# Performance work log

Hardware: AMD Instinct MI355X
Metric: run time of the kernel (lower is better)

## Reference

```python
import jax, jax.numpy as jnp
import numpy as np

CONF_THRES = 0.25
IOU_THRES = 0.45
MAX_DET = 300
K_NMS = 2048          # static candidate cap for jit-compatible NMS
MAX_WH = 7680.0       # yolov5 class-offset trick for non-agnostic NMS
IN_H, IN_W = 640.0, 640.0     # network input size (self.size)
OUT_H, OUT_W = 1080.0, 1920.0  # original frame size (h, w)


def setup_inputs() -> dict:
    key = jax.random.key(0)
    k1, k2, k3, k4 = jax.random.split(key, 4)
    bs, n, nc = 16, 25200, 80
    # realistic raw yolov5 head output: xywh in pixels, obj/cls in [0,1]
    xy = jax.random.uniform(k1, (bs, n, 2), jnp.float32) * 640.0
    wh = jax.random.uniform(k2, (bs, n, 2), jnp.float32) * 120.0 + 2.0
    obj = jax.random.uniform(k3, (bs, n, 1), jnp.float32)
    cls = jax.random.uniform(k4, (bs, n, nc), jnp.float32)
    preds = jnp.concatenate([xy, wh, obj, cls], axis=-1)  # [bs, 25200, 85]
    return {"preds": preds}


def _xywh2xyxy(x):
    xy, wh = x[..., :2], x[..., 2:4]
    return jnp.concatenate([xy - wh * 0.5, xy + wh * 0.5], axis=-1)


def _iou_one_many(b, boxes):
    # b: [4], boxes: [K,4] (xyxy) -> [K]
    lt = jnp.maximum(b[:2], boxes[:, :2])
    rb = jnp.minimum(b[2:], boxes[:, 2:])
    wh = jnp.clip(rb - lt, 0.0)
    inter = wh[:, 0] * wh[:, 1]
    a1 = (b[2] - b[0]) * (b[3] - b[1])
    a2 = (boxes[:, 2] - boxes[:, 0]) * (boxes[:, 3] - boxes[:, 1])
    return inter / (a1 + a2 - inter + 1e-7)


def _nms_sorted(boxes, valid):
    # boxes [K,4] sorted by score desc (class-offset applied); valid [K] bool
    K = boxes.shape[0]
    idxs = jnp.arange(K)

    def step(suppressed, i):
        keep_i = valid[i] & jnp.logical_not(suppressed[i])
        iou = _iou_one_many(boxes[i], boxes)  # [K]
        suppressed = suppressed | (keep_i & (iou > IOU_THRES) & (idxs > i))
        return suppressed, keep_i

    _, keep = jax.lax.scan(step, jnp.zeros((K,), bool), idxs)
    # first MAX_DET kept indices (stable: preserves score order)
    sel = jnp.argsort(jnp.logical_not(keep), stable=True)[:MAX_DET]
    return sel, keep[sel]


def reference(preds):
    # --- yolov5 non_max_suppression (multi_label=False, agnostic=False) ---
    obj = preds[..., 4:5]                      # [bs,N,1]
    cls_conf = preds[..., 5:] * obj            # conf = obj * cls
    conf = jnp.max(cls_conf, axis=-1)          # [bs,N]
    cls = jnp.argmax(cls_conf, axis=-1)        # [bs,N] int
    mask = (preds[..., 4] > CONF_THRES) & (conf > CONF_THRES)
    score = jnp.where(mask, conf, -1.0)

    top_s, top_i = jax.lax.top_k(score, K_NMS)                      # [bs,K]
    cand_xywh = jnp.take_along_axis(preds[..., :4], top_i[..., None], axis=1)
    cand_boxes = _xywh2xyxy(cand_xywh)                              # [bs,K,4]
    cand_cls = jnp.take_along_axis(cls, top_i, axis=1)              # [bs,K]
    valid = top_s > 0.0

    boxes_off = cand_boxes + cand_cls[..., None].astype(cand_boxes.dtype) * MAX_WH
    sel, keep = jax.vmap(_nms_sorted)(boxes_off, valid)             # [bs,MAX_DET]

    det_boxes = jnp.take_along_axis(cand_boxes, sel[..., None], axis=1)
    det_scores = jnp.take_along_axis(top_s, sel, axis=1)
    det_cls = jnp.take_along_axis(cand_cls, sel, axis=1)

    # --- scale_bbox: (640,640) -> (h,w) original frame ---
    scale = jnp.array([OUT_W / IN_W, OUT_H / IN_H, OUT_W / IN_W, OUT_H / IN_H],
                      dtype=det_boxes.dtype)
    det_boxes = det_boxes * scale

    det = jnp.concatenate(
        [det_boxes, det_scores[..., None], det_cls[..., None].astype(det_boxes.dtype)],
        axis=-1)                                                    # [bs,MAX_DET,6]
    det = jnp.where(keep[..., None], det, 0.0)
    return det
```

## Files before the change

### kernel.cpp

```cpp
#include <hip/hip_runtime.h>
#include <stdint.h>

#define BS 16
#define NP 25200
#define NC 80
#define DIM 85
#define KN 2048
#define CAP 4096
#define BINS 512
#define MAXD 300
#define NBLK 394

__global__ __launch_bounds__(256) void score_kernel(const float* __restrict__ preds,
        float* __restrict__ score, int* __restrict__ clsout) {
    int b = blockIdx.x / NBLK;
    int blk = blockIdx.x % NBLK;
    int i0 = blk * 64;
    int nb = min(64, NP - i0);
    __shared__ float4 s4[64 * DIM / 4];
    const float4* p4 = (const float4*)(preds + ((size_t)b * NP + i0) * DIM);
    int tot4 = (nb * DIM) >> 2;
    float4 tmp[6];
    #pragma unroll
    for (int kx = 0; kx < 6; ++kx) {
        int idx = kx * 256 + threadIdx.x;
        tmp[kx] = (idx < tot4) ? p4[idx] : make_float4(0.f, 0.f, 0.f, 0.f);
    }
    #pragma unroll
    for (int kx = 0; kx < 6; ++kx) {
        int idx = kx * 256 + threadIdx.x;
        if (idx < tot4) s4[idx] = tmp[kx];
    }
    __syncthreads();
    const float* s = (const float*)s4;
    int box = threadIdx.x >> 2, sub = threadIdx.x & 3;
    if (box < nb) {
        const float* bp = s + box * DIM;
        float obj = bp[4];
        float best = -1.0f; int bidx = sub * 20;
        #pragma unroll
        for (int c = 0; c < 20; ++c) {
            float v = bp[5 + sub * 20 + c] * obj;
            if (v > best) { best = v; bidx = sub * 20 + c; }
        }
        #pragma unroll
        for (int off = 1; off < 4; off <<= 1) {
            float ob = __shfl_xor(best, off);
            int   oi = __shfl_xor(bidx, off);
            if (ob > best || (ob == best && oi < bidx)) { best = ob; bidx = oi; }
        }
        if (sub == 0) {
            bool m = (obj > 0.25f) && (best > 0.25f);
            int gi = b * NP + i0 + box;
            score[gi] = m ? best : -1.0f;
            clsout[gi] = bidx;
        }
    }
}

template<int V, bool DESC, typename T>
__device__ inline void wave_bitonic(T (&v)[V], int lane) {
    const int N = V * 64;
    #pragma unroll
    for (int k = 2; k <= N; k <<= 1) {
        #pragma unroll
        for (int j = N >> 1; j > 0; j >>= 1) {
            if (j >= k) continue;
            if (j >= 64) {
                int dv = j >> 6;
                #pragma unroll
                for (int a = 0; a < V; ++a) {
                    int p = a ^ dv;
                    if (a < p) {
                        int e = a * 64;
                        bool kml = (((e & k) == 0) == DESC);
                        T lo = v[a], hi = v[p];
                        T mx = lo > hi ? lo : hi;
                        T mn = lo > hi ? hi : lo;
                        v[a] = kml ? mx : mn;
                        v[p] = kml ? mn : mx;
                    }
                }
            } else {
                #pragma unroll
                for (int a = 0; a < V; ++a) {
                    int e = a * 64 + lane;
                    T pv = __shfl_xor(v[a], j);
                    bool isLower = (lane & j) == 0;
                    bool kml = (((e & k) == 0) == DESC);
                    bool takeMax = (kml == isLower);
                    T mx = v[a] > pv ? v[a] : pv;
                    T mn = v[a] > pv ? pv : v[a];
                    v[a] = takeMax ? mx : mn;
                }
            }
        }
    }
}

__global__ __launch_bounds__(1024) void sort_kernel(
        const float* __restrict__ score, const float* __restrict__ preds,
        const int* __restrict__ cls,
        unsigned long long* __restrict__ gkeys, float4* __restrict__ gboxes,
        int* __restrict__ gcarr, unsigned short* __restrict__ gcorder,
        int* __restrict__ gcstart, int* __restrict__ gccnt,
        unsigned char* __restrict__ keepG) {
    int b = blockIdx.x;
    int tid = threadIdx.x;
    int lane = tid & 63;
    int wid = tid >> 6;

    __shared__ unsigned long long k[CAP];
    __shared__ int h[BINS];
    __shared__ int bstartA[BINS];
    __shared__ int bcnt[BINS];
    __shared__ int carr[KN];
    __shared__ unsigned short corder[KN];
    __shared__ int sT;

    for (int t = tid; t < BINS; t += 1024) { h[t] = 0; bcnt[t] = 0; }
    __syncthreads();
    const float* sb = score + (size_t)b * NP;
    for (int i = tid; i < NP; i += 1024) {
        float v = sb[i];
        if (v > 0.0f) {
            int bin = (int)(__float_as_uint(v) >> 15) - 0x7D00;
            bin = max(0, min(BINS - 1, bin));
            atomicAdd(&h[bin], 1);
        }
    }
    __syncthreads();
    if (tid < 64) {
        int base = lane * 8;
        int v[8]; int ssum = 0;
        #pragma unroll
        for (int kk = 0; kk < 8; ++kk) { v[kk] = h[base + kk]; ssum += v[kk]; }
        int x = ssum;
        #pragma unroll
        for (int off = 1; off < 64; off <<= 1) {
            int y = __shfl_down(x, off);
            if (lane + off < 64) x += y;
        }
        int run = x - ssum;
        int cand = -1;
        #pragma unroll
        for (int kk = 7; kk >= 0; --kk) {
            bstartA[base + kk] = run;
            run += v[kk];
            if (run >= KN && cand < 0) cand = base + kk;
        }
        #pragma unroll
        for (int off = 1; off < 64; off <<= 1) cand = max(cand, __shfl_xor(cand, off));
        if (lane == 0) sT = max(cand, 0);
    }
    __syncthreads();
    int T = sT;
    int n = min(bstartA[T] + h[T], CAP);
    int Mb = min(n, KN);
    for (int i = tid; i < NP; i += 1024) {
        float sc = sb[i];
        if (sc > 0.0f) {
            int bin = (int)(__float_as_uint(sc) >> 15) - 0x7D00;
            bin = max(0, min(BINS - 1, bin));
            if (bin >= T) {
                int pos = bstartA[bin] + atomicAdd(&bcnt[bin], 1);
                if (pos < CAP) {
                    unsigned int ii = (unsigned int)i;
                    k[pos] = ((unsigned long long)__float_as_uint(sc) << 32)
                           | (unsigned int)(~ii);
                }
            }
        }
    }
    __syncthreads();
    for (int bin = (T & ~15) + wid; bin < BINS; bin += 16) {
        if (bin < T) continue;
        int cnt = h[bin];
        if (cnt <= 0) continue;
        int bs = bstartA[bin];
        unsigned long long v[4];
        #pragma unroll
        for (int a = 0; a < 4; ++a) {
            int idx = a * 64 + lane;
            v[a] = (idx < cnt && bs + idx < CAP) ? k[bs + idx] : 0ull;
        }
        wave_bitonic<4, true>(v, lane);
        #pragma unroll
        for (int a = 0; a < 4; ++a) {
            int idx = a * 64 + lane;
            if (idx < cnt && bs + idx < CAP) k[bs + idx] = v[a];
        }
    }
    __syncthreads();
    for (int r = tid; r < KN; r += 1024) {
        keepG[b * KN + r] = 0;
        if (r < Mb) {
            unsigned long long key = k[r];
            unsigned int i = ~(unsigned int)key;
            const float* p = preds + ((size_t)b * NP + i) * DIM;
            float x = p[0], y = p[1], w = p[2], hh = p[3];
            float4 bx = make_float4(x - w * 0.5f, y - hh * 0.5f,
                                    x + w * 0.5f, y + hh * 0.5f);
            int c = cls[(size_t)b * NP + i];
            gboxes[b * KN + r] = bx;
            gkeys [b * KN + r] = key;
            gcarr [b * KN + r] = c;
            carr[r] = c;
        }
    }
    if (tid < 128) { h[tid] = 0; bcnt[tid] = 0; }
    __syncthreads();
    for (int r = tid; r < Mb; r += 1024) atomicAdd(&h[carr[r]], 1);
    __syncthreads();
    if (tid < 64) {
        int a = h[lane];
        int sa = a;
        #pragma unroll
        for (int off = 1; off < 64; off <<= 1) {
            int y = __shfl_up(sa, off);
            if (lane >= off) sa += y;
        }
        bstartA[lane] = sa - a;
        int tot64 = __shfl(sa, 63);
        int b2 = (lane < 16) ? h[64 + lane] : 0;
        int sb2 = b2;
        #pragma unroll
        for (int off = 1; off < 64; off <<= 1) {
            int y = __shfl_up(sb2, off);
            if (lane >= off) sb2 += y;
        }
        if (lane < 16) bstartA[64 + lane] = tot64 + (sb2 - b2);
    }
    __syncthreads();
    for (int r = tid; r < Mb; r += 1024) {
        int c = carr[r];
        int pos = bstartA[c] + atomicAdd(&bcnt[c], 1);
        corder[pos] = (unsigned short)r;
    }
    __syncthreads();
    #pragma unroll
    for (int t5 = 0; t5 < 5; ++t5) {
        int c = wid + 16 * t5;
        int nc = h[c];
        int bs = bstartA[c];
        if (nc > 0) {
            unsigned int v[2];
            v[0] = (lane < nc) ? (unsigned int)corder[bs + lane] : 0xFFFFFFFFu;
            v[1] = (lane + 64 < nc) ? (unsigned int)corder[bs + 64 + lane] : 0xFFFFFFFFu;
            wave_bitonic<2, false>(v, lane);
            if (lane < nc) corder[bs + lane] = (unsigned short)v[0];
            if (lane + 64 < nc) corder[bs + 64 + lane] = (unsigned short)v[1];
        }
    }
    __syncthreads();
    for (int t = tid; t < Mb; t += 1024) gcorder[b * KN + t] = corder[t];
    if (tid < NC) { gcstart[b * NC + tid] = bstartA[tid]; gccnt[b * NC + tid] = h[tid]; }
}

__global__ __launch_bounds__(64) void nms_kernel(const float4* __restrict__ gboxes,
        const unsigned short* __restrict__ gcorder, const int* __restrict__ gcstart,
        const int* __restrict__ gccnt, unsigned char* __restrict__ keepG) {
    int b = blockIdx.x / NC;
    int c = blockIdx.x % NC;
    int nc = gccnt[b * NC + c];
    if (nc <= 0) return;
    int bs = gcstart[b * NC + c];
    int lane = threadIdx.x;
    int ord0 = (lane < nc) ? (int)gcorder[b * KN + bs + lane] : 0;
    int ord1 = (lane + 64 < nc) ? (int)gcorder[b * KN + bs + 64 + lane] : 0;
    float4 A0 = (lane < nc) ? gboxes[b * KN + ord0] : make_float4(0.f, 0.f, 0.f, 0.f);
    float4 A1 = (lane + 64 < nc) ? gboxes[b * KN + ord1] : make_float4(0.f, 0.f, 0.f, 0.f);
    float off = (float)c * 7680.0f;
    A0.x += off; A0.y += off; A0.z += off; A0.w += off;
    A1.x += off; A1.y += off; A1.z += off; A1.w += off;
    float ar0 = (A0.z - A0.x) * (A0.w - A0.y);
    float ar1 = (A1.z - A1.x) * (A1.w - A1.y);
    unsigned long long sup0 = 0, sup1 = 0, keep0 = 0, keep1 = 0;
    for (int idx = 0; idx < nc; ++idx) {
        bool hi = idx >= 64;
        int bit = idx & 63;
        unsigned long long s = hi ? sup1 : sup0;
        if ((s >> bit) & 1ull) continue;
        if (hi) keep1 |= 1ull << bit; else keep0 |= 1ull << bit;
        float bx_ = hi ? __shfl(A1.x, bit) : __shfl(A0.x, bit);
        float by_ = hi ? __shfl(A1.y, bit) : __shfl(A0.y, bit);
        float bz_ = hi ? __shfl(A1.z, bit) : __shfl(A0.z, bit);
        float bw_ = hi ? __shfl(A1.w, bit) : __shfl(A0.w, bit);
        float ba_ = hi ? __shfl(ar1, bit) : __shfl(ar0, bit);
        bool s0, s1;
        {
            float lx = fmaxf(bx_, A0.x), ly = fmaxf(by_, A0.y);
            float rx = fminf(bz_, A0.z), ry = fminf(bw_, A0.w);
            float iw = fmaxf(rx - lx, 0.0f), ih = fmaxf(ry - ly, 0.0f);
            float inter = iw * ih;
            float iou = inter / (ba_ + ar0 - inter + 1e-7f);
            s0 = (lane > idx) && (lane < nc) && (iou > 0.45f);
        }
        {
            float lx = fmaxf(bx_, A1.x), ly = fmaxf(by_, A1.y);
            float rx = fminf(bz_, A1.z), ry = fminf(bw_, A1.w);
            float iw = fmaxf(rx - lx, 0.0f), ih = fmaxf(ry - ly, 0.0f);
            float inter = iw * ih;
            float iou = inter / (ba_ + ar1 - inter + 1e-7f);
            s1 = ((64 + lane) > idx) && ((64 + lane) < nc) && (iou > 0.45f);
        }
        sup0 |= __ballot(s0);
        sup1 |= __ballot(s1);
    }
    if (lane < nc && ((keep0 >> lane) & 1ull)) keepG[b * KN + ord0] = 1;
    if (lane + 64 < nc && ((keep1 >> lane) & 1ull)) keepG[b * KN + ord1] = 1;
}

__global__ __launch_bounds__(64) void out_kernel(const unsigned char* __restrict__ keepG,
        const unsigned long long* __restrict__ gkeys, const float4* __restrict__ gboxes,
        const int* __restrict__ gcarr, float* __restrict__ out) {
    int b = blockIdx.x;
    int lane = threadIdx.x;
    int running = 0;
    for (int ch = 0; ch < 32; ++ch) {
        int r = ch * 64 + lane;
        bool kp = keepG[b * KN + r] != 0;
        unsigned long long m = __ballot(kp);
        int pos = running + (int)__popcll(m & ((1ull << lane) - 1ull));
        if (kp && pos < MAXD) {
            float4 bx = gboxes[b * KN + r];
            float sc = __uint_as_float((unsigned int)(gkeys[b * KN + r] >> 32));
            float* o = out + ((size_t)b * MAXD + pos) * 6;
            o[0] = bx.x * 3.0f;
            o[1] = bx.y * 1.6875f;
            o[2] = bx.z * 3.0f;
            o[3] = bx.w * 1.6875f;
            o[4] = sc;
            o[5] = (float)gcarr[b * KN + r];
        }
        running += (int)__popcll(m);
    }
}

extern "C" void kernel_launch(void* const* d_in, const int* in_sizes, int n_in,
                              void* d_out, int out_size, void* d_ws, size_t ws_size,
                              hipStream_t stream) {
    const float* preds = (const float*)d_in[0];
    float* out = (float*)d_out;
    char* ws = (char*)d_ws;
    size_t off = 0;
    auto alloc = [&](size_t bytes) -> void* {
        void* p = ws + off;
        off += (bytes + 255) & ~(size_t)255;
        return p;
    };
    float* score = (float*)alloc((size_t)BS * NP * 4);
    int* cls    = (int*)alloc((size_t)BS * NP * 4);
    unsigned long long* gkeys = (unsigned long long*)alloc((size_t)BS * KN * 8);
    float4* gboxes = (float4*)alloc((size_t)BS * KN * 16);
    int* gcarr  = (int*)alloc((size_t)BS * KN * 4);
    unsigned short* gcorder = (unsigned short*)alloc((size_t)BS * KN * 2);
    int* gcstart = (int*)alloc((size_t)BS * NC * 4);
    int* gccnt   = (int*)alloc((size_t)BS * NC * 4);
    unsigned char* keepG = (unsigned char*)alloc((size_t)BS * KN);
    if (ws_size < off) return;

    hipMemsetAsync(d_out, 0, (size_t)out_size * 4, stream);

    score_kernel<<<BS * NBLK, 256, 0, stream>>>(preds, score, cls);
    sort_kernel<<<BS, 1024, 0, stream>>>(score, preds, cls, gkeys, gboxes,
            gcarr, gcorder, gcstart, gccnt, keepG);
    nms_kernel<<<BS * NC, 64, 0, stream>>>(gboxes, gcorder, gcstart, gccnt, keepG);
    out_kernel<<<BS, 64, 0, stream>>>(keepG, gkeys, gboxes, gcarr, out);
}
```

Baseline: 292.8 us.

## Split sort stage across many blocks and fuse histogram into score kernel

The score kernel now computes the per-chunk score histogram and skips the class scan when objectness is below threshold. It also drops the shared-memory staging in favour of one thread per box. The single-block-per-image sort is split: a light kernel does the prefix and scatter to global keys, and a new multi-block kernel bitonic-sorts each bin and builds boxes. The per-class ordering moves into the NMS kernel, which compacts its own class members with a ballot scan. The aim is to remove the serial, low-occupancy 16-block sort bottleneck, at the cost of an extra launch, more global traffic, and uncoalesced per-thread strided reads of preds.

```diff
diff --git a/kernel.cpp b/kernel.cpp
--- a/kernel.cpp
+++ b/kernel.cpp
@@ -9,53 +9,50 @@
 #define CAP 4096
 #define BINS 512
 #define MAXD 300
-#define NBLK 394
-
-__global__ __launch_bounds__(256) void score_kernel(const float* __restrict__ preds,
-        float* __restrict__ score, int* __restrict__ clsout) {
-    int b = blockIdx.x / NBLK;
-    int blk = blockIdx.x % NBLK;
-    int i0 = blk * 64;
-    int nb = min(64, NP - i0);
-    __shared__ float4 s4[64 * DIM / 4];
-    const float4* p4 = (const float4*)(preds + ((size_t)b * NP + i0) * DIM);
-    int tot4 = (nb * DIM) >> 2;
-    float4 tmp[6];
-    #pragma unroll
-    for (int kx = 0; kx < 6; ++kx) {
-        int idx = kx * 256 + threadIdx.x;
-        tmp[kx] = (idx < tot4) ? p4[idx] : make_float4(0.f, 0.f, 0.f, 0.f);
-    }
-    #pragma unroll
-    for (int kx = 0; kx < 6; ++kx) {
-        int idx = kx * 256 + threadIdx.x;
-        if (idx < tot4) s4[idx] = tmp[kx];
-    }
-    __syncthreads();
-    const float* s = (const float*)s4;
-    int box = threadIdx.x >> 2, sub = threadIdx.x & 3;
-    if (box < nb) {
-        const float* bp = s + box * DIM;
+#define SBLK 99
+#define QCAP 128
+
+__global__ __launch_bounds__(256) void score_hist_kernel(const float* __restrict__ preds,
+        float* __restrict__ score, int* __restrict__ clsout, int* __restrict__ hpart) {
+    int b = blockIdx.x / SBLK;
+    int chunk = blockIdx.x % SBLK;
+    int tid = threadIdx.x;
+    __shared__ int h[BINS];
+    h[tid] = 0; h[tid + 256] = 0;
+    __syncthreads();
+    int n = chunk * 256 + tid;
+    if (n < NP) {
+        const float* bp = preds + ((size_t)b * NP + n) * DIM;
         float obj = bp[4];
-        float best = -1.0f; int bidx = sub * 20;
-        #pragma unroll
-        for (int c = 0; c < 20; ++c) {
-            float v = bp[5 + sub * 20 + c] * obj;
-            if (v > best) { best = v; bidx = sub * 20 + c; }
-        }
-        #pragma unroll
-        for (int off = 1; off < 4; off <<= 1) {
-            float ob = __shfl_xor(best, off);
-            int   oi = __shfl_xor(bidx, off);
-            if (ob > best || (ob == best && oi < bidx)) { best = ob; bidx = oi; }
-        }
-        if (sub == 0) {
-            bool m = (obj > 0.25f) && (best > 0.25f);
-            int gi = b * NP + i0 + box;
-            score[gi] = m ? best : -1.0f;
-            clsout[gi] = bidx;
-        }
-    }
+        float sc = -1.0f; int bidx = 0;
+        if (obj > 0.25f) {
+            float best = -1.0f;
+            #pragma unroll
+            for (int kk = 0; kk < 10; ++kk) {
+                float v[8];
+                #pragma unroll
+                for (int j = 0; j < 8; ++j) v[j] = bp[5 + kk * 8 + j];
+                #pragma unroll
+                for (int j = 0; j < 8; ++j) {
+                    float s = v[j] * obj;
+                    if (s > best) { best = s; bidx = kk * 8 + j; }
+                }
+            }
+            if (best > 0.25f) sc = best;
+        }
+        int gi = b * NP + n;
+        score[gi] = sc;
+        clsout[gi] = bidx;
+        if (sc > 0.0f) {
+            int bin = (int)(__float_as_uint(sc) >> 15) - 0x7D00;
+            bin = max(0, min(BINS - 1, bin));
+            atomicAdd(&h[bin], 1);
+        }
+    }
+    __syncthreads();
+    int* hp = hpart + ((size_t)(b * SBLK + chunk)) * BINS;
+    hp[tid] = h[tid];
+    hp[tid + 256] = h[tid + 256];
 }
 
 template<int V, bool DESC, typename T>
@@ -98,36 +95,24 @@
     }
 }
 
-__global__ __launch_bounds__(1024) void sort_kernel(
-        const float* __restrict__ score, const float* __restrict__ preds,
-        const int* __restrict__ cls,
-        unsigned long long* __restrict__ gkeys, float4* __restrict__ gboxes,
-        int* __restrict__ gcarr, unsigned short* __restrict__ gcorder,
-        int* __restrict__ gcstart, int* __restrict__ gccnt,
-        unsigned char* __restrict__ keepG) {
+__global__ __launch_bounds__(1024) void sort16_kernel(const float* __restrict__ score,
+        const int* __restrict__ hpart,
+        unsigned long long* __restrict__ gkeys, int* __restrict__ gmeta,
+        int* __restrict__ gbstart, int* __restrict__ gcnt,
+        unsigned char* __restrict__ carrU8, unsigned char* __restrict__ keepG) {
     int b = blockIdx.x;
     int tid = threadIdx.x;
     int lane = tid & 63;
-    int wid = tid >> 6;
-
-    __shared__ unsigned long long k[CAP];
     __shared__ int h[BINS];
     __shared__ int bstartA[BINS];
     __shared__ int bcnt[BINS];
-    __shared__ int carr[KN];
-    __shared__ unsigned short corder[KN];
     __shared__ int sT;
-
-    for (int t = tid; t < BINS; t += 1024) { h[t] = 0; bcnt[t] = 0; }
-    __syncthreads();
-    const float* sb = score + (size_t)b * NP;
-    for (int i = tid; i < NP; i += 1024) {
-        float v = sb[i];
-        if (v > 0.0f) {
-            int bin = (int)(__float_as_uint(v) >> 15) - 0x7D00;
-            bin = max(0, min(BINS - 1, bin));
-            atomicAdd(&h[bin], 1);
-        }
+    if (tid < BINS) {
+        int s = 0;
+        const int* hp = hpart + ((size_t)b * SBLK) * BINS + tid;
+        for (int c = 0; c < SBLK; ++c) s += hp[c * BINS];
+        h[tid] = s;
+        bcnt[tid] = 0;
     }
     __syncthreads();
     if (tid < 64) {
@@ -157,6 +142,7 @@
     int T = sT;
     int n = min(bstartA[T] + h[T], CAP);
     int Mb = min(n, KN);
+    const float* sb = score + (size_t)b * NP;
     for (int i = tid; i < NP; i += 1024) {
         float sc = sb[i];
         if (sc > 0.0f) {
@@ -166,108 +152,86 @@
                 int pos = bstartA[bin] + atomicAdd(&bcnt[bin], 1);
                 if (pos < CAP) {
                     unsigned int ii = (unsigned int)i;
-                    k[pos] = ((unsigned long long)__float_as_uint(sc) << 32)
-                           | (unsigned int)(~ii);
+                    gkeys[(size_t)b * CAP + pos] =
+                        ((unsigned long long)__float_as_uint(sc) << 32)
+                        | (unsigned int)(~ii);
                 }
             }
         }
     }
-    __syncthreads();
-    for (int bin = (T & ~15) + wid; bin < BINS; bin += 16) {
-        if (bin < T) continue;
-        int cnt = h[bin];
+    for (int r = tid; r < KN; r += 1024) { keepG[b * KN + r] = 0; carrU8[b * KN + r] = 0xFF; }
+    if (tid < BINS) { gbstart[b * BINS + tid] = bstartA[tid]; gcnt[b * BINS + tid] = h[tid]; }
+    if (tid == 0) { gmeta[2 * b] = T; gmeta[2 * b + 1] = Mb; }
+}
+
+__global__ __launch_bounds__(256) void binsort_build_kernel(const float* __restrict__ preds,
+        const int* __restrict__ cls, unsigned long long* __restrict__ gkeys,
+        const int* __restrict__ gmeta, const int* __restrict__ gbstart,
+        const int* __restrict__ gcnt,
+        float4* __restrict__ gboxes, unsigned char* __restrict__ carrU8) {
+    int b = blockIdx.x >> 5;
+    int g = blockIdx.x & 31;
+    int lane = threadIdx.x & 63;
+    int wv = threadIdx.x >> 6;
+    int T = gmeta[2 * b];
+    int Mb = gmeta[2 * b + 1];
+    int wslot = g * 4 + wv;
+    for (int bin = T + wslot; bin < BINS; bin += 128) {
+        int cnt = gcnt[b * BINS + bin];
         if (cnt <= 0) continue;
-        int bs = bstartA[bin];
+        int bs = gbstart[b * BINS + bin];
+        if (bs >= Mb) continue;
         unsigned long long v[4];
         #pragma unroll
         for (int a = 0; a < 4; ++a) {
             int idx = a * 64 + lane;
-            v[a] = (idx < cnt && bs + idx < CAP) ? k[bs + idx] : 0ull;
+            v[a] = (idx < cnt && bs + idx < CAP) ? gkeys[(size_t)b * CAP + bs + idx] : 0ull;
         }
         wave_bitonic<4, true>(v, lane);
         #pragma unroll
         for (int a = 0; a < 4; ++a) {
             int idx = a * 64 + lane;
-            if (idx < cnt && bs + idx < CAP) k[bs + idx] = v[a];
-        }
-    }
-    __syncthreads();
-    for (int r = tid; r < KN; r += 1024) {
-        keepG[b * KN + r] = 0;
-        if (r < Mb) {
-            unsigned long long key = k[r];
-            unsigned int i = ~(unsigned int)key;
-            const float* p = preds + ((size_t)b * NP + i) * DIM;
-            float x = p[0], y = p[1], w = p[2], hh = p[3];
-            float4 bx = make_float4(x - w * 0.5f, y - hh * 0.5f,
-                                    x + w * 0.5f, y + hh * 0.5f);
-            int c = cls[(size_t)b * NP + i];
-            gboxes[b * KN + r] = bx;
-            gkeys [b * KN + r] = key;
-            gcarr [b * KN + r] = c;
-            carr[r] = c;
-        }
-    }
-    if (tid < 128) { h[tid] = 0; bcnt[tid] = 0; }
-    __syncthreads();
-    for (int r = tid; r < Mb; r += 1024) atomicAdd(&h[carr[r]], 1);
-    __syncthreads();
-    if (tid < 64) {
-        int a = h[lane];
-        int sa = a;
-        #pragma unroll
-        for (int off = 1; off < 64; off <<= 1) {
-            int y = __shfl_up(sa, off);
-            if (lane >= off) sa += y;
-        }
-        bstartA[lane] = sa - a;
-        int tot64 = __shfl(sa, 63);
-        int b2 = (lane < 16) ? h[64 + lane] : 0;
-        int sb2 = b2;
-        #pragma unroll
-        for (int off = 1; off < 64; off <<= 1) {
-            int y = __shfl_up(sb2, off);
-            if (lane >= off) sb2 += y;
-        }
-        if (lane < 16) bstartA[64 + lane] = tot64 + (sb2 - b2);
-    }
-    __syncthreads();
-    for (int r = tid; r < Mb; r += 1024) {
-        int c = carr[r];
-        int pos = bstartA[c] + atomicAdd(&bcnt[c], 1);
-        corder[pos] = (unsigned short)r;
-    }
-    __syncthreads();
-    #pragma unroll
-    for (int t5 = 0; t5 < 5; ++t5) {
-        int c = wid + 16 * t5;
-        int nc = h[c];
-        int bs = bstartA[c];
-        if (nc > 0) {
-            unsigned int v[2];
-            v[0] = (lane < nc) ? (unsigned int)corder[bs + lane] : 0xFFFFFFFFu;
-            v[1] = (lane + 64 < nc) ? (unsigned int)corder[bs + 64 + lane] : 0xFFFFFFFFu;
-            wave_bitonic<2, false>(v, lane);
-            if (lane < nc) corder[bs + lane] = (unsigned short)v[0];
-            if (lane + 64 < nc) corder[bs + 64 + lane] = (unsigned short)v[1];
-        }
-    }
-    __syncthreads();
-    for (int t = tid; t < Mb; t += 1024) gcorder[b * KN + t] = corder[t];
-    if (tid < NC) { gcstart[b * NC + tid] = bstartA[tid]; gccnt[b * NC + tid] = h[tid]; }
+            if (idx < cnt && bs + idx < CAP) gkeys[(size_t)b * CAP + bs + idx] = v[a];
+        }
+        #pragma unroll
+        for (int a = 0; a < 4; ++a) {
+            int idx = a * 64 + lane;
+            int r = bs + idx;
+            if (idx < cnt && r < Mb) {
+                unsigned long long key = v[a];
+                unsigned int i = ~(unsigned int)key;
+                const float* p = preds + ((size_t)b * NP + i) * DIM;
+                float x = p[0], y = p[1], w = p[2], hh = p[3];
+                gboxes[b * KN + r] = make_float4(x - w * 0.5f, y - hh * 0.5f,
+                                                x + w * 0.5f, y + hh * 0.5f);
+                carrU8[b * KN + r] = (unsigned char)cls[(size_t)b * NP + i];
+            }
+        }
+    }
 }
 
 __global__ __launch_bounds__(64) void nms_kernel(const float4* __restrict__ gboxes,
-        const unsigned short* __restrict__ gcorder, const int* __restrict__ gcstart,
-        const int* __restrict__ gccnt, unsigned char* __restrict__ keepG) {
+        const unsigned char* __restrict__ carrU8, const int* __restrict__ gmeta,
+        unsigned char* __restrict__ keepG) {
     int b = blockIdx.x / NC;
     int c = blockIdx.x % NC;
-    int nc = gccnt[b * NC + c];
+    int lane = threadIdx.x;
+    int Mb = gmeta[2 * b + 1];
+    __shared__ unsigned short q[QCAP];
+    int base = 0;
+    for (int r0 = 0; r0 < Mb; r0 += 64) {
+        int r = r0 + lane;
+        bool mine = (r < Mb) && (carrU8[b * KN + r] == (unsigned char)c);
+        unsigned long long m = __ballot(mine);
+        int pos = base + (int)__popcll(m & ((1ull << lane) - 1ull));
+        if (mine && pos < QCAP) q[pos] = (unsigned short)r;
+        base += (int)__popcll(m);
+    }
+    __syncthreads();
+    int nc = min(base, QCAP);
     if (nc <= 0) return;
-    int bs = gcstart[b * NC + c];
-    int lane = threadIdx.x;
-    int ord0 = (lane < nc) ? (int)gcorder[b * KN + bs + lane] : 0;
-    int ord1 = (lane + 64 < nc) ? (int)gcorder[b * KN + bs + 64 + lane] : 0;
+    int ord0 = (lane < nc) ? (int)q[lane] : 0;
+    int ord1 = (lane + 64 < nc) ? (int)q[64 + lane] : 0;
     float4 A0 = (lane < nc) ? gboxes[b * KN + ord0] : make_float4(0.f, 0.f, 0.f, 0.f);
     float4 A1 = (lane + 64 < nc) ? gboxes[b * KN + ord1] : make_float4(0.f, 0.f, 0.f, 0.f);
     float off = (float)c * 7680.0f;
@@ -313,7 +277,7 @@
 
 __global__ __launch_bounds__(64) void out_kernel(const unsigned char* __restrict__ keepG,
         const unsigned long long* __restrict__ gkeys, const float4* __restrict__ gboxes,
-        const int* __restrict__ gcarr, float* __restrict__ out) {
+        const unsigned char* __restrict__ carrU8, float* __restrict__ out) {
     int b = blockIdx.x;
     int lane = threadIdx.x;
     int running = 0;
@@ -324,14 +288,14 @@
         int pos = running + (int)__popcll(m & ((1ull << lane) - 1ull));
         if (kp && pos < MAXD) {
             float4 bx = gboxes[b * KN + r];
-            float sc = __uint_as_float((unsigned int)(gkeys[b * KN + r] >> 32));
+            float sc = __uint_as_float((unsigned int)(gkeys[(size_t)b * CAP + r] >> 32));
             float* o = out + ((size_t)b * MAXD + pos) * 6;
             o[0] = bx.x * 3.0f;
             o[1] = bx.y * 1.6875f;
             o[2] = bx.z * 3.0f;
             o[3] = bx.w * 1.6875f;
             o[4] = sc;
-            o[5] = (float)gcarr[b * KN + r];
+            o[5] = (float)carrU8[b * KN + r];
         }
         running += (int)__popcll(m);
     }
@@ -351,20 +315,23 @@
     };
     float* score = (float*)alloc((size_t)BS * NP * 4);
     int* cls    = (int*)alloc((size_t)BS * NP * 4);
-    unsigned long long* gkeys = (unsigned long long*)alloc((size_t)BS * KN * 8);
+    int* hpart  = (int*)alloc((size_t)BS * SBLK * BINS * 4);
+    unsigned long long* gkeys = (unsigned long long*)alloc((size_t)BS * CAP * 8);
     float4* gboxes = (float4*)alloc((size_t)BS * KN * 16);
-    int* gcarr  = (int*)alloc((size_t)BS * KN * 4);
-    unsigned short* gcorder = (unsigned short*)alloc((size_t)BS * KN * 2);
-    int* gcstart = (int*)alloc((size_t)BS * NC * 4);
-    int* gccnt   = (int*)alloc((size_t)BS * NC * 4);
-    unsigned char* keepG = (unsigned char*)alloc((size_t)BS * KN);
+    unsigned char* carrU8 = (unsigned char*)alloc((size_t)BS * KN);
+    unsigned char* keepG  = (unsigned char*)alloc((size_t)BS * KN);
+    int* gmeta   = (int*)alloc(BS * 2 * 4);
+    int* gbstart = (int*)alloc((size_t)BS * BINS * 4);
+    int* gcnt    = (int*)alloc((size_t)BS * BINS * 4);
     if (ws_size < off) return;
 
     hipMemsetAsync(d_out, 0, (size_t)out_size * 4, stream);
 
-    score_kernel<<<BS * NBLK, 256, 0, stream>>>(preds, score, cls);
-    sort_kernel<<<BS, 1024, 0, stream>>>(score, preds, cls, gkeys, gboxes,
-            gcarr, gcorder, gcstart, gccnt, keepG);
-    nms_kernel<<<BS * NC, 64, 0, stream>>>(gboxes, gcorder, gcstart, gccnt, keepG);
-    out_kernel<<<BS, 64, 0, stream>>>(keepG, gkeys, gboxes, gcarr, out);
-}
+    score_hist_kernel<<<BS * SBLK, 256, 0, stream>>>(preds, score, cls, hpart);
+    sort16_kernel<<<BS, 1024, 0, stream>>>(score, hpart, gkeys, gmeta, gbstart, gcnt,
+                                           carrU8, keepG);
+    binsort_build_kernel<<<BS * 32, 256, 0, stream>>>(preds, cls, gkeys, gmeta,
+                                                      gbstart, gcnt, gboxes, carrU8);
+    nms_kernel<<<BS * NC, 64, 0, stream>>>(gboxes, carrU8, gmeta, keepG);
+    out_kernel<<<BS, 64, 0, stream>>>(keepG, gkeys, gboxes, carrU8, out);
+}
```

Result: faster. 262.5 us (-10.4%).
